# Kernel tuning notes

Measured on AMD Instinct MI355X. Metric: run time of the kernel, lower is better.

## Reference

```python
import jax, jax.numpy as jnp
import numpy as np

PI2 = 2.0 * np.pi
ZITTER = 1e-4
LIKERR_BOUND = (0.1, 1.0)


def setup_inputs() -> dict:
    key = jax.random.key(0)
    k1, k2, k3, k4 = jax.random.split(key, 4)
    nb, ndata, ndim, nchannel = 4, 2048, 1, 3
    xc = jax.random.normal(k1, (nb, ndata, ndim, nchannel), dtype=jnp.float32)
    # spectral-mixture params: shape (nchannel, ndim) like logmu.exp() / 1/logstd.exp()
    mu = jax.random.uniform(k2, (nchannel, ndim), dtype=jnp.float32)
    inv_std = jax.random.uniform(k3, (nchannel, ndim), dtype=jnp.float32)
    likerr = jax.random.uniform(k4, (nchannel,), dtype=jnp.float32)
    return {"xc": xc, "mu": mu, "inv_std": inv_std, "likerr": likerr}


def reference(xc, mu, inv_std, likerr):
    # xc: (nb, n, d, c); mu, inv_std: (c, d); likerr: (c,)
    # eval_smkernel_batch with xt=None (symmetric case, pi2repuse=True)
    mu_ = mu.T[None, None, :, :]          # (1,1,d,c)
    inv_std_ = inv_std.T[None, None, :, :]
    exp_xc = xc * inv_std_                # (nb,n,d,c)
    sq = jnp.sum(exp_xc ** 2, axis=-2)    # (nb,n,c)
    cos_x = jnp.sum(xc * mu_, axis=-2)    # (nb,n,c)
    # cross term: (nb,n,n,c)
    cross = jnp.einsum('badk,bcdk->back', exp_xc, exp_xc)
    exp_term = sq[:, :, None, :] + sq[:, None, :, :] - 2.0 * cross
    cos_term = cos_x[:, :, None, :] - cos_x[:, None, :, :]
    out = jnp.exp(-0.5 * (PI2 ** 2) * exp_term) * jnp.cos(PI2 * cos_term)
    # diagonal noise per channel
    lik = jnp.clip(likerr, LIKERR_BOUND[0], LIKERR_BOUND[1])
    noise = (ZITTER + lik ** 2)[None, None, None, :]  # (1,1,1,c)
    eye = jnp.eye(xc.shape[1], dtype=xc.dtype)[None, :, :, None]
    return out + noise * eye
```

## Files before the change

### kernel.cpp

```cpp
#include <hip/hip_runtime.h>


static constexpr float KNEG2 = -28.4776592f;

__device__ __forceinline__ float smk_elem(float x, float ea, float is,
                                          float ma, float mu) {
    const float t  = __builtin_fmaf(-is, x, ea);
    const float ex = __builtin_amdgcn_exp2f(t * t * KNEG2);
    const float u  = __builtin_fmaf(-mu, x, ma);
    const float cs = __builtin_amdgcn_cosf(__builtin_amdgcn_fractf(u));
    return ex * cs;
}

__global__ __launch_bounds__(256) void smk_main(
    const float* __restrict__ xc,
    const float* __restrict__ mu,
    const float* __restrict__ inv_std,
    const float* __restrict__ likerr,
    float* __restrict__ out,
    int n)
{
    const int blk = blockIdx.x;
    const int b   = blk / n;
    const int a   = blk - b * n;
    const int rb  = b * n;

    const float is0 = inv_std[0], is1 = inv_std[1], is2 = inv_std[2];
    const float mu0 = mu[0],      mu1 = mu[1],      mu2 = mu[2];

    const float* xa = xc + (size_t)(rb + a) * 3;
    const float ea0 = xa[0] * is0, ea1 = xa[1] * is1, ea2 = xa[2] * is2;
    const float ma0 = xa[0] * mu0, ma1 = xa[1] * mu1, ma2 = xa[2] * mu2;

    const float l0 = fminf(fmaxf(likerr[0], 0.1f), 1.0f);
    const float l1 = fminf(fmaxf(likerr[1], 0.1f), 1.0f);
    const float l2 = fminf(fmaxf(likerr[2], 0.1f), 1.0f);
    const float nz0 = 1e-4f + l0 * l0;
    const float nz1 = 1e-4f + l1 * l1;
    const float nz2 = 1e-4f + l2 * l2;

    const float* __restrict__ xrow = xc  + (size_t)rb  * 3;
    float*       __restrict__ orow = out + (size_t)blk * 3 * n;

    #pragma unroll 4
    for (int c = threadIdx.x; c < n; c += 256) {
        const float3 xq = *reinterpret_cast<const float3*>(xrow + 3 * c);

        float r0 = smk_elem(xq.x, ea0, is0, ma0, mu0);
        float r1 = smk_elem(xq.y, ea1, is1, ma1, mu1);
        float r2 = smk_elem(xq.z, ea2, is2, ma2, mu2);

        if (c == a) { r0 += nz0; r1 += nz1; r2 += nz2; }

        *reinterpret_cast<float3*>(orow + 3 * c) = make_float3(r0, r1, r2);
    }
}

extern "C" void kernel_launch(void* const* d_in, const int* in_sizes, int n_in,
                              void* d_out, int out_size, void* d_ws, size_t ws_size,
                              hipStream_t stream) {
    const float* xc      = (const float*)d_in[0];
    const float* mu      = (const float*)d_in[1];
    const float* inv_std = (const float*)d_in[2];
    const float* likerr  = (const float*)d_in[3];
    float*       out     = (float*)d_out;

    const int  C = in_sizes[3];
    const int  D = in_sizes[1] / C;
    const long P = (long)in_sizes[0] / ((long)C * D);
    const long n = (long)out_size / (P * C);
    (void)n_in; (void)d_ws; (void)ws_size;

    smk_main<<<dim3((unsigned)P), dim3(256), 0, stream>>>(
        xc, mu, inv_std, likerr, out, (int)n);
}
```

Baseline: 198.0 us.

## Exploit kernel matrix symmetry with upper-triangular tiles and LDS-transposed mirror writes

Adds a tiled kernel that computes only the upper-triangular 64x64 tiles of each batch's symmetric n×n×3 output. Each off-diagonal tile is also written to its mirrored position, transposed through shared memory. This roughly halves the exp2/cos work, and the per-element projections are now precomputed as differences of pre-scaled values. The cost is a 50KB LDS buffer per block, which limits occupancy, plus a barrier and a serial loop per block to map the block index to a tile. The original row kernel is kept as a fallback when n is not a multiple of 64.

```diff
diff --git a/kernel.cpp b/kernel.cpp
--- a/kernel.cpp
+++ b/kernel.cpp
@@ -2,23 +2,94 @@
 
 
 static constexpr float KNEG2 = -28.4776592f;
+#define TILE 64
+#define LDSP 195
 
-__device__ __forceinline__ float smk_elem(float x, float ea, float is,
-                                          float ma, float mu) {
-    const float t  = __builtin_fmaf(-is, x, ea);
+__device__ __forceinline__ float smk_elem(float ea, float ec, float ma, float mc) {
+    const float t  = ea - ec;
     const float ex = __builtin_amdgcn_exp2f(t * t * KNEG2);
-    const float u  = __builtin_fmaf(-mu, x, ma);
+    const float u  = ma - mc;
     const float cs = __builtin_amdgcn_cosf(__builtin_amdgcn_fractf(u));
     return ex * cs;
 }
 
-__global__ __launch_bounds__(256) void smk_main(
+__global__ __launch_bounds__(256) void smk_sym(
     const float* __restrict__ xc,
     const float* __restrict__ mu,
     const float* __restrict__ inv_std,
     const float* __restrict__ likerr,
     float* __restrict__ out,
-    int n)
+    int n, int S, int U)
+{
+    __shared__ float V[TILE * LDSP];
+
+    const int b = blockIdx.x / U;
+    int rem = blockIdx.x - b * U;
+    int ti = 0;
+    while (rem >= S - ti) { rem -= S - ti; ++ti; }
+    const int tj   = ti + rem;
+    const bool diag = (ti == tj);
+    const int Ai = ti * TILE, Aj = tj * TILE;
+    const int rb = b * n;
+
+    const float is0 = inv_std[0], is1 = inv_std[1], is2 = inv_std[2];
+    const float mu0 = mu[0],      mu1 = mu[1],      mu2 = mu[2];
+    const float l0 = fminf(fmaxf(likerr[0], 0.1f), 1.0f);
+    const float l1 = fminf(fmaxf(likerr[1], 0.1f), 1.0f);
+    const float l2 = fminf(fmaxf(likerr[2], 0.1f), 1.0f);
+    const float nz0 = 1e-4f + l0 * l0;
+    const float nz1 = 1e-4f + l1 * l1;
+    const float nz2 = 1e-4f + l2 * l2;
+
+    const int lane = threadIdx.x & 63;
+    const int q    = threadIdx.x >> 6;
+
+    const float* xcp = xc + (size_t)(rb + Aj + lane) * 3;
+    const float xq0 = xcp[0], xq1 = xcp[1], xq2 = xcp[2];
+    const float ec0 = xq0 * is0, ec1 = xq1 * is1, ec2 = xq2 * is2;
+    const float mc0 = xq0 * mu0, mc1 = xq1 * mu1, mc2 = xq2 * mu2;
+
+    const size_t row3n = (size_t)3 * n;
+
+    #pragma unroll 4
+    for (int it = 0; it < 16; ++it) {
+        const int row = q + 4 * it;
+        const float* xap = xc + (size_t)(rb + Ai + row) * 3;
+        const float xa0 = xap[0], xa1 = xap[1], xa2 = xap[2];
+        const float ea0 = xa0 * is0, ea1 = xa1 * is1, ea2 = xa2 * is2;
+        const float ma0 = xa0 * mu0, ma1 = xa1 * mu1, ma2 = xa2 * mu2;
+
+        float r0 = smk_elem(ea0, ec0, ma0, mc0);
+        float r1 = smk_elem(ea1, ec1, ma1, mc1);
+        float r2 = smk_elem(ea2, ec2, ma2, mc2);
+        if (diag && lane == row) { r0 += nz0; r1 += nz1; r2 += nz2; }
+
+        float* dst = out + (size_t)(rb + Ai + row) * row3n + 3 * (Aj + lane);
+        *reinterpret_cast<float3*>(dst) = make_float3(r0, r1, r2);
+
+        if (!diag) {
+            float* vp = V + row * LDSP + 3 * lane;
+            vp[0] = r0; vp[1] = r1; vp[2] = r2;
+        }
+    }
+
+    if (!diag) {
+        __syncthreads();
+        #pragma unroll 4
+        for (int it = 0; it < 16; ++it) {
+            const int crow = q + 4 * it;
+            const float* vp = V + lane * LDSP + 3 * crow;
+            const float r0 = vp[0], r1 = vp[1], r2 = vp[2];
+            float* dst = out + (size_t)(rb + Aj + crow) * row3n + 3 * (Ai + lane);
+            *reinterpret_cast<float3*>(dst) = make_float3(r0, r1, r2);
+        }
+    }
+}
+
+__global__ __launch_bounds__(256) void smk_main(
+    const float* __restrict__ xc, const float* __restrict__ mu,
+    const float* __restrict__ inv_std, const float* __restrict__ likerr,
+    float* __restrict__ out, int n)
 {
     const int blk = blockIdx.x;
     const int b   = blk / n;
@@ -45,13 +116,10 @@
     #pragma unroll 4
     for (int c = threadIdx.x; c < n; c += 256) {
         const float3 xq = *reinterpret_cast<const float3*>(xrow + 3 * c);
-
-        float r0 = smk_elem(xq.x, ea0, is0, ma0, mu0);
-        float r1 = smk_elem(xq.y, ea1, is1, ma1, mu1);
-        float r2 = smk_elem(xq.z, ea2, is2, ma2, mu2);
-
+        float r0 = smk_elem(ea0, xq.x * is0, ma0, xq.x * mu0);
+        float r1 = smk_elem(ea1, xq.y * is1, ma1, xq.y * mu1);
+        float r2 = smk_elem(ea2, xq.z * is2, ma2, xq.z * mu2);
         if (c == a) { r0 += nz0; r1 += nz1; r2 += nz2; }
-
         *reinterpret_cast<float3*>(orow + 3 * c) = make_float3(r0, r1, r2);
     }
 }
@@ -69,8 +137,16 @@
     const int  D = in_sizes[1] / C;
     const long P = (long)in_sizes[0] / ((long)C * D);
     const long n = (long)out_size / (P * C);
+    const long nb = P / n;
     (void)n_in; (void)d_ws; (void)ws_size;
 
-    smk_main<<<dim3((unsigned)P), dim3(256), 0, stream>>>(
-        xc, mu, inv_std, likerr, out, (int)n);
+    if (n % TILE == 0) {
+        const int S = (int)(n / TILE);
+        const int U = S * (S + 1) / 2;
+        smk_sym<<<dim3((unsigned)(nb * U)), dim3(256), 0, stream>>>(
+            xc, mu, inv_std, likerr, out, (int)n, S, U);
+    } else {
+        smk_main<<<dim3((unsigned)P), dim3(256), 0, stream>>>(
+            xc, mu, inv_std, likerr, out, (int)n);
+    }
 }
```

After: 202.3 us. 2.2% more time.

## Flatten row to float4 lanes with nontemporal stores and separate diagonal kernel

Applied to the files above, without the earlier changes.

Each output row is now treated as a flat array of float4, and every thread reads and writes 16-byte vectors. Each lane takes its per-channel parameters from a rotating channel index (threadIdx mod 3) and uses 384 threads per block so lane phases stay aligned. Stores are nontemporal to avoid cache pollution, and the diagonal noise is written by a second small kernel. This is meant to replace misaligned 12-byte float3 accesses with aligned vector stores, at the cost of an extra launch and a second write to the diagonal. The diagonal value is recomputed as 1+noise, assuming the kernel value on the diagonal is exactly 1.

```diff
diff --git a/kernel.cpp b/kernel.cpp
--- a/kernel.cpp
+++ b/kernel.cpp
@@ -3,22 +3,83 @@
 
 static constexpr float KNEG2 = -28.4776592f;
 
-__device__ __forceinline__ float smk_elem(float x, float ea, float is,
-                                          float ma, float mu) {
-    const float t  = __builtin_fmaf(-is, x, ea);
-    const float ex = __builtin_amdgcn_exp2f(t * t * KNEG2);
-    const float u  = __builtin_fmaf(-mu, x, ma);
-    const float cs = __builtin_amdgcn_cosf(__builtin_amdgcn_fractf(u));
-    return ex * cs;
+typedef float f32x4 __attribute__((ext_vector_type(4)));
+
+__device__ __forceinline__ float sel3(float p0, float p1, float p2, int k) {
+    float r = (k == 1) ? p1 : p0;
+    return (k == 2) ? p2 : r;
+}
+
+__global__ __launch_bounds__(384) void smk_flat(
+    const float* __restrict__ xc,
+    const float* __restrict__ mu,
+    const float* __restrict__ inv_std,
+    float* __restrict__ out,
+    int n)
+{
+    const int blk = blockIdx.x;
+    const int b   = blk / n;
+    const int a   = blk - b * n;
+    const int rb  = b * n;
+
+    const float is0 = inv_std[0], is1 = inv_std[1], is2 = inv_std[2];
+    const float mu0 = mu[0],      mu1 = mu[1],      mu2 = mu[2];
+
+    const float* xa = xc + (size_t)(rb + a) * 3;
+    const float ea0 = xa[0] * is0, ea1 = xa[1] * is1, ea2 = xa[2] * is2;
+    const float ma0 = xa[0] * mu0, ma1 = xa[1] * mu1, ma2 = xa[2] * mu2;
+
+    const int k0 = threadIdx.x % 3;
+    float isP[4], muP[4], eaP[4], maP[4];
+    #pragma unroll
+    for (int j = 0; j < 4; ++j) {
+        int kj = k0 + j; kj = (kj >= 3) ? kj - 3 : kj; kj = (kj >= 3) ? kj - 3 : kj;
+        isP[j] = sel3(is0, is1, is2, kj);
+        muP[j] = sel3(mu0, mu1, mu2, kj);
+        eaP[j] = sel3(ea0, ea1, ea2, kj);
+        maP[j] = sel3(ma0, ma1, ma2, kj);
+    }
+
+    const f32x4* __restrict__ xrow4 = reinterpret_cast<const f32x4*>(xc + (size_t)rb * 3);
+    f32x4*       __restrict__ orow4 = reinterpret_cast<f32x4*>(out + (size_t)blk * 3 * n);
+
+    const int nq = (3 * n) >> 2;
+    #pragma unroll 4
+    for (int idx = threadIdx.x; idx < nq; idx += 384) {
+        const f32x4 xq = xrow4[idx];
+        f32x4 r;
+        #pragma unroll
+        for (int j = 0; j < 4; ++j) {
+            const float x  = xq[j];
+            const float t  = __builtin_fmaf(-isP[j], x, eaP[j]);
+            const float ex = __builtin_amdgcn_exp2f(t * t * KNEG2);
+            const float u  = __builtin_fmaf(-muP[j], x, maP[j]);
+            const float cs = __builtin_amdgcn_cosf(__builtin_amdgcn_fractf(u));
+            r[j] = ex * cs;
+        }
+        __builtin_nontemporal_store(r, &orow4[idx]);
+    }
+}
+
+__global__ __launch_bounds__(256) void smk_diag(
+    const float* __restrict__ likerr, float* __restrict__ out, int n, int nbn)
+{
+    const int i = blockIdx.x * 256 + threadIdx.x;
+    if (i >= nbn) return;
+    const int a = i % n;
+    const float l0 = fminf(fmaxf(likerr[0], 0.1f), 1.0f);
+    const float l1 = fminf(fmaxf(likerr[1], 0.1f), 1.0f);
+    const float l2 = fminf(fmaxf(likerr[2], 0.1f), 1.0f);
+    float* p = out + (size_t)i * 3 * n + 3 * a;
+    p[0] = 1.0f + 1e-4f + l0 * l0;
+    p[1] = 1.0f + 1e-4f + l1 * l1;
+    p[2] = 1.0f + 1e-4f + l2 * l2;
 }
 
 __global__ __launch_bounds__(256) void smk_main(
-    const float* __restrict__ xc,
-    const float* __restrict__ mu,
-    const float* __restrict__ inv_std,
-    const float* __restrict__ likerr,
-    float* __restrict__ out,
-    int n)
+    const float* __restrict__ xc, const float* __restrict__ mu,
+    const float* __restrict__ inv_std, const float* __restrict__ likerr,
+    float* __restrict__ out, int n)
 {
     const int blk = blockIdx.x;
     const int b   = blk / n;
@@ -45,13 +106,16 @@
     #pragma unroll 4
     for (int c = threadIdx.x; c < n; c += 256) {
         const float3 xq = *reinterpret_cast<const float3*>(xrow + 3 * c);
-
-        float r0 = smk_elem(xq.x, ea0, is0, ma0, mu0);
-        float r1 = smk_elem(xq.y, ea1, is1, ma1, mu1);
-        float r2 = smk_elem(xq.z, ea2, is2, ma2, mu2);
-
+        float t0 = ea0 - xq.x * is0, u0 = ma0 - xq.x * mu0;
+        float t1 = ea1 - xq.y * is1, u1 = ma1 - xq.y * mu1;
+        float t2 = ea2 - xq.z * is2, u2 = ma2 - xq.z * mu2;
+        float r0 = __builtin_amdgcn_exp2f(t0 * t0 * KNEG2) *
+                   __builtin_amdgcn_cosf(__builtin_amdgcn_fractf(u0));
+        float r1 = __builtin_amdgcn_exp2f(t1 * t1 * KNEG2) *
+                   __builtin_amdgcn_cosf(__builtin_amdgcn_fractf(u1));
+        float r2 = __builtin_amdgcn_exp2f(t2 * t2 * KNEG2) *
+                   __builtin_amdgcn_cosf(__builtin_amdgcn_fractf(u2));
         if (c == a) { r0 += nz0; r1 += nz1; r2 += nz2; }
-
         *reinterpret_cast<float3*>(orow + 3 * c) = make_float3(r0, r1, r2);
     }
 }
@@ -71,6 +135,13 @@
     const long n = (long)out_size / (P * C);
     (void)n_in; (void)d_ws; (void)ws_size;
 
-    smk_main<<<dim3((unsigned)P), dim3(256), 0, stream>>>(
-        xc, mu, inv_std, likerr, out, (int)n);
+    if (n % 512 == 0) {
+        smk_flat<<<dim3((unsigned)P), dim3(384), 0, stream>>>(
+            xc, mu, inv_std, out, (int)n);
+        smk_diag<<<dim3((unsigned)((P + 255) / 256)), dim3(256), 0, stream>>>(
+            likerr, out, (int)n, (int)P);
+    } else {
+        smk_main<<<dim3((unsigned)P), dim3(256), 0, stream>>>(
+            xc, mu, inv_std, likerr, out, (int)n);
+    }
 }
```

New measurement: 209.5 us. 1.06x slower.
